# Performance work log

Measured on AMD Instinct MI355X. Metric: run time of the kernel, lower is better.

Reference implementation:

```python
import jax, jax.numpy as jnp
import numpy as np

B, L, D, H = 2, 2048, 1024, 16
HD = D // H
NEG = -1000000000.0


def setup_inputs() -> dict:
    key = jax.random.key(0)
    ks = jax.random.split(key, 11)
    s = 1.0 / np.sqrt(D)
    return {
        "q": jax.random.normal(ks[0], (B, L, D), jnp.float32),
        "k": jax.random.normal(ks[1], (B, L, D), jnp.float32),
        "v": jax.random.normal(ks[2], (B, L, D), jnp.float32),
        "mask": jnp.ones((B, L, L), jnp.int32),
        "Wq": jax.random.normal(ks[3], (D, D), jnp.float32) * s,
        "bq": jnp.zeros((D,), jnp.float32),
        "Wk": jax.random.normal(ks[4], (D, D), jnp.float32) * s,
        "bk": jnp.zeros((D,), jnp.float32),
        "Wv": jax.random.normal(ks[5], (D, D), jnp.float32) * s,
        "bv": jnp.zeros((D,), jnp.float32),
        "Wo": jax.random.normal(ks[6], (D, D), jnp.float32) * s,
        "bo": jnp.zeros((D,), jnp.float32),
    }


def _split(x):
    # [B,L,D] -> [B,H,L,HD]
    return x.reshape(B, L, H, HD).transpose(0, 2, 1, 3)


def reference(q, k, v, mask, Wq, bq, Wk, bk, Wv, bv, Wo, bo):
    Q = _split(q @ Wq.T + bq)
    K = _split(k @ Wk.T + bk)
    V = _split(v @ Wv.T + bv)
    scores = jnp.einsum("bhqd,bhkd->bhqk", Q, K) / jnp.sqrt(jnp.float32(HD))
    m = mask[:, None, :, :]  # [B,1,L,L]
    scores = jnp.where(m == 0, NEG, scores)
    attn = jax.nn.softmax(scores, axis=-1)
    out = jnp.einsum("bhqk,bhkd->bhqd", attn, V)
    out = out.transpose(0, 2, 1, 3).reshape(B, L, D)
    out = out @ Wo.T + bo
    return out, attn
```

## Files before the change

kernel.cpp:

```cpp
#include <hip/hip_runtime.h>
#include <stdint.h>

#define BSZ 2
#define LSEQ 2048
#define DMOD 1024
#define NH 16
#define HDSZ 64
#define NT (LSEQ / 128)

typedef __attribute__((ext_vector_type(8))) short short8;
typedef __attribute__((ext_vector_type(4))) float f32x4;
typedef __attribute__((ext_vector_type(4))) unsigned short u16x4;
typedef __attribute__((ext_vector_type(4))) int i32x4;

#define MFMA16(a, b, c) __builtin_amdgcn_mfma_f32_16x16x32_bf16((a), (b), (c), 0, 0, 0)
#define EXP2F(x) __builtin_amdgcn_exp2f(x)

__device__ __forceinline__ unsigned short f2bf(float f) {
  union { float f; unsigned u; } x; x.f = f;
  unsigned u = x.u + 0x7fffu + ((x.u >> 16) & 1u);
  return (unsigned short)(u >> 16);
}

__device__ __forceinline__ unsigned cvt_pk_bf16(float lo, float hi) {
  unsigned r;
  asm("v_cvt_pk_bf16_f32 %0, %1, %2" : "=v"(r) : "v"(lo), "v"(hi));
  return r;
}

__device__ __forceinline__ short8 pack8(f32x4 lo, f32x4 hi) {
  short8 o;
  o[0] = f2bf(lo[0]); o[1] = f2bf(lo[1]); o[2] = f2bf(lo[2]); o[3] = f2bf(lo[3]);
  o[4] = f2bf(hi[0]); o[5] = f2bf(hi[1]); o[6] = f2bf(hi[2]); o[7] = f2bf(hi[3]);
  return o;
}

template <int AF32, int OUTF32>
__global__ __launch_bounds__(256) void gemm_bt(
    const void* __restrict__ A0, const void* __restrict__ A1, const void* __restrict__ A2,
    const float* __restrict__ W0, const float* __restrict__ W1, const float* __restrict__ W2,
    const float* __restrict__ b0, const float* __restrict__ b1, const float* __restrict__ b2,
    void* __restrict__ C0, void* __restrict__ C1, void* __restrict__ C2,
    float s0, float s1, float s2, int vtz, int M, int N, int K,
    const int* __restrict__ mask, int* __restrict__ flags) {
  const int z = blockIdx.z;
  const int tid = threadIdx.x;
  __shared__ int red[4];

  if (z == 3) {
    const int t0 = (blockIdx.x + 32 * blockIdx.y) * 2;
#pragma unroll
    for (int t = t0; t < t0 + 2; ++t) {
      const int b_ = t >> 8, qt = (t >> 4) & 15, ktt = t & 15;
      const int r = tid >> 1, c = (tid & 1) * 64;
      const int* mr = mask + (size_t)b_ * LSEQ * LSEQ + (size_t)(qt * 128 + r) * LSEQ +
                      ktt * 128 + c;
      int ok = 1;
#pragma unroll
      for (int j = 0; j < 16; j++) {
        i32x4 v = __builtin_nontemporal_load((const i32x4*)(mr + j * 4));
        ok &= (v[0] != 0) & (v[1] != 0) & (v[2] != 0) & (v[3] != 0);
      }
      unsigned long long vote = __ballot(ok);
      if ((tid & 63) == 0) red[tid >> 6] = (vote == ~0ull) ? 1 : 0;
      __syncthreads();
      if (tid == 0) flags[(b_ * 16 + qt) * 16 + ktt] = red[0] & red[1] & red[2] & red[3];
      __syncthreads();
    }
    return;
  }

  const void* A = (z == 0) ? A0 : ((z == 1) ? A1 : A2);
  const float* W = (z == 0) ? W0 : ((z == 1) ? W1 : W2);
  const float* bias = (z == 0) ? b0 : ((z == 1) ? b1 : b2);
  void* Cout = (z == 0) ? C0 : ((z == 1) ? C1 : C2);
  const float scale = (z == 0) ? s0 : ((z == 1) ? s1 : s2);

  __shared__ unsigned short As[128 * 40];
  __shared__ unsigned short Bs[128 * 40];

  const int lane = tid & 63;
  const int wid = tid >> 6;
  const int bm = blockIdx.x, bn = blockIdx.y;
  const int wm = (wid >> 1) * 64, wn = (wid & 1) * 64;

  f32x4 acc[4][4];
#pragma unroll
  for (int i = 0; i < 4; i++)
#pragma unroll
    for (int j = 0; j < 4; j++) acc[i][j] = (f32x4){0.f, 0.f, 0.f, 0.f};

  const int r0 = tid >> 2;
  const int c0 = (tid & 3) * 8;
  const float* Wg = W + (size_t)(bn * 128 + r0) * K + c0;

  f32x4 vaf[2][2], vbf[2][2];
  short8 vah[2];
  if constexpr (AF32) {
    const float* Ag = (const float*)A + (size_t)(bm * 128 + r0) * K + c0;
#pragma unroll
    for (int j = 0; j < 2; j++) {
      vaf[j][0] = *(const f32x4*)(Ag + (size_t)(j * 64) * K);
      vaf[j][1] = *(const f32x4*)(Ag + (size_t)(j * 64) * K + 4);
    }
  } else {
    const unsigned short* Ag = (const unsigned short*)A + (size_t)(bm * 128 + r0) * K + c0;
#pragma unroll
    for (int j = 0; j < 2; j++) vah[j] = *(const short8*)(Ag + (size_t)(j * 64) * K);
  }
#pragma unroll
  for (int j = 0; j < 2; j++) {
    vbf[j][0] = *(const f32x4*)(Wg + (size_t)(j * 64) * K);
    vbf[j][1] = *(const f32x4*)(Wg + (size_t)(j * 64) * K + 4);
  }

  for (int k0 = 0; k0 < K; k0 += 32) {
#pragma unroll
    for (int j = 0; j < 2; j++) {
      if constexpr (AF32)
        *(short8*)&As[(j * 64 + r0) * 40 + c0] = pack8(vaf[j][0], vaf[j][1]);
      else
        *(short8*)&As[(j * 64 + r0) * 40 + c0] = vah[j];
      *(short8*)&Bs[(j * 64 + r0) * 40 + c0] = pack8(vbf[j][0], vbf[j][1]);
    }
    __syncthreads();
    if (k0 + 32 < K) {
      if constexpr (AF32) {
        const float* Ag = (const float*)A + (size_t)(bm * 128 + r0) * K + c0 + k0 + 32;
#pragma unroll
        for (int j = 0; j < 2; j++) {
          vaf[j][0] = *(const f32x4*)(Ag + (size_t)(j * 64) * K);
          vaf[j][1] = *(const f32x4*)(Ag + (size_t)(j * 64) * K + 4);
        }
      } else {
        const unsigned short* Ag =
            (const unsigned short*)A + (size_t)(bm * 128 + r0) * K + c0 + k0 + 32;
#pragma unroll
        for (int j = 0; j < 2; j++) vah[j] = *(const short8*)(Ag + (size_t)(j * 64) * K);
      }
#pragma unroll
      for (int j = 0; j < 2; j++) {
        vbf[j][0] = *(const f32x4*)(Wg + (size_t)(j * 64) * K + k0 + 32);
        vbf[j][1] = *(const f32x4*)(Wg + (size_t)(j * 64) * K + k0 + 36);
      }
    }
    short8 af[4], bf[4];
#pragma unroll
    for (int i = 0; i < 4; i++)
      af[i] = *(const short8*)&As[(wm + i * 16 + (lane & 15)) * 40 + (lane >> 4) * 8];
#pragma unroll
    for (int i = 0; i < 4; i++)
      bf[i] = *(const short8*)&Bs[(wn + i * 16 + (lane & 15)) * 40 + (lane >> 4) * 8];
#pragma unroll
    for (int i = 0; i < 4; i++)
#pragma unroll
      for (int j = 0; j < 4; j++) acc[i][j] = MFMA16(af[i], bf[j], acc[i][j]);
    __syncthreads();
  }

  const bool vtrans = (z == vtz);
  const int crow = bm * 128 + wm + ((lane >> 4) & 3) * 4;
#pragma unroll
  for (int j = 0; j < 4; j++) {
    const int col = bn * 128 + wn + j * 16 + (lane & 15);
    const float bv = bias[col];
#pragma unroll
    for (int i = 0; i < 4; i++) {
      if (OUTF32) {
#pragma unroll
        for (int r = 0; r < 4; r++) {
          float vvv = (acc[i][j][r] + bv) * scale;
          ((float*)Cout)[(size_t)(crow + i * 16 + r) * N + col] = vvv;
        }
      } else if (vtrans) {
        u16x4 pk;
#pragma unroll
        for (int r = 0; r < 4; r++) pk[r] = f2bf((acc[i][j][r] + bv) * scale);
        const int row = crow + i * 16;
        unsigned short* dst = (unsigned short*)Cout +
                              (size_t)(row >> 11) * DMOD * LSEQ + (size_t)col * LSEQ +
                              (row & (LSEQ - 1));
        *(u16x4*)dst = pk;
      } else {
#pragma unroll
        for (int r = 0; r < 4; r++) {
          float vvv = (acc[i][j][r] + bv) * scale;
          ((unsigned short*)Cout)[(size_t)(crow + i * 16 + r) * N + col] = f2bf(vvv);
        }
      }
    }
  }
}

__global__ __launch_bounds__(256) void attn_kernel(
    const unsigned short* __restrict__ Qp, const unsigned short* __restrict__ Kp,
    const unsigned short* __restrict__ Vt, const int* __restrict__ mask,
    const int* __restrict__ flags, float* __restrict__ attn_out,
    unsigned short* __restrict__ ctx) {
  __shared__ unsigned short Ks[4][64 * 64];
  __shared__ unsigned short Ps[4][64][68];
  __shared__ float denbuf[2][128];

  const int tid = threadIdx.x, lane = tid & 63, wid = tid >> 6;
  const int kw = wid & 1, qw = wid >> 1;
  const int l15 = lane & 15, lg = lane >> 4;

  const int wgid = blockIdx.x + gridDim.x * blockIdx.y;
  const int jj = wgid >> 3;
  const int bh = (wgid & 7) * 4 + (jj >> 4);
  const int qt = jj & 15;
  const int q0 = qt * 128;
  const int b = bh >> 4, h = bh & 15;

  const unsigned short* Qh = Qp + (size_t)b * LSEQ * DMOD + h * HDSZ;
  const unsigned short* Kh = Kp + (size_t)b * LSEQ * DMOD + h * HDSZ;
  const unsigned short* Vh = Vt + (size_t)b * DMOD * LSEQ + (size_t)h * HDSZ * LSEQ;
  const int* mb = mask + (size_t)b * LSEQ * LSEQ;
  const int* frow = flags + (b * 16 + qt) * 16;
  float* ah = attn_out + (size_t)bh * LSEQ * LSEQ;

  const int wq0 = q0 + qw * 64;
  const int wk0 = kw * 64;

  short8 qf[4][2];
#pragma unroll
  for (int fq = 0; fq < 4; fq++)
#pragma unroll
    for (int ks = 0; ks < 2; ks++)
      qf[fq][ks] = *(const short8*)(Qh + (size_t)(wq0 + fq * 16 + l15) * DMOD +
                                    ks * 32 + lg * 8);

  unsigned short* Ksw = &Ks[wid][0];
  const int rl8 = lane >> 3, jc = lane & 7;
  const unsigned short* Kwb = Kh + (size_t)(wk0 + rl8) * DMOD + jc * 8;

  float den[4] = {0.f, 0.f, 0.f, 0.f};
  short8 ka[8];
#pragma unroll
  for (int p = 0; p < 8; p++) ka[p] = *(const short8*)(Kwb + (size_t)(p * 8) * DMOD);

  for (int kt = 0; kt < NT; ++kt) {
#pragma unroll
    for (int p = 0; p < 8; p++) {
      const int r = p * 8 + rl8;
      *(short8*)&Ksw[r * 64 + ((jc ^ (r & 7)) << 3)] = ka[p];
    }
    if (kt + 1 < NT) {
#pragma unroll
      for (int p = 0; p < 8; p++)
        ka[p] = *(const short8*)(Kwb + (size_t)((kt + 1) * 128 + p * 8) * DMOD);
    }
    const bool fast = frow[kt] != 0;
    if (fast) {
#pragma unroll
      for (int fn = 0; fn < 4; fn++) {
        const int krow = fn * 16 + l15;
        const int rb = krow * 64, rx = (krow & 7) << 4;
        short8 kf0 = *(const short8*)&Ksw[rb + (((lg * 16) ^ rx) >> 1)];
        short8 kf1 = *(const short8*)&Ksw[rb + (((64 + lg * 16) ^ rx) >> 1)];
#pragma unroll
        for (int fq = 0; fq < 4; fq++) {
          f32x4 s = (f32x4){0.f, 0.f, 0.f, 0.f};
          s = MFMA16(kf0, qf[fq][0], s);
          s = MFMA16(kf1, qf[fq][1], s);
          den[fq] += EXP2F(s[0]) + EXP2F(s[1]) + EXP2F(s[2]) + EXP2F(s[3]);
        }
      }
    } else {
      const int k0 = kt * 128;
#pragma unroll
      for (int fn = 0; fn < 4; fn++) {
        const int krow = fn * 16 + l15;
        const int rb = krow * 64, rx = (krow & 7) << 4;
        short8 kf0 = *(const short8*)&Ksw[rb + (((lg * 16) ^ rx) >> 1)];
        short8 kf1 = *(const short8*)&Ksw[rb + (((64 + lg * 16) ^ rx) >> 1)];
#pragma unroll
        for (int fq = 0; fq < 4; fq++) {
          const int qrow = wq0 + fq * 16 + l15;
          f32x4 s = (f32x4){0.f, 0.f, 0.f, 0.f};
          s = MFMA16(kf0, qf[fq][0], s);
          s = MFMA16(kf1, qf[fq][1], s);
          i32x4 m4 = *(const i32x4*)(mb + (size_t)qrow * LSEQ + k0 + wk0 + fn * 16 + lg * 4);
          den[fq] += (m4[0] != 0) ? EXP2F(s[0]) : 0.f;
          den[fq] += (m4[1] != 0) ? EXP2F(s[1]) : 0.f;
          den[fq] += (m4[2] != 0) ? EXP2F(s[2]) : 0.f;
          den[fq] += (m4[3] != 0) ? EXP2F(s[3]) : 0.f;
        }
      }
    }
  }
#pragma unroll
  for (int fq = 0; fq < 4; fq++) {
    den[fq] += __shfl_xor(den[fq], 16);
    den[fq] += __shfl_xor(den[fq], 32);
  }
  if (lg == 0) {
#pragma unroll
    for (int fq = 0; fq < 4; fq++) denbuf[kw][qw * 64 + fq * 16 + l15] = den[fq];
  }
  __syncthreads();
  float inv[4];
#pragma unroll
  for (int fq = 0; fq < 4; fq++) {
    const int ql = qw * 64 + fq * 16 + l15;
    inv[fq] = 1.0f / (denbuf[0][ql] + denbuf[1][ql]);
  }

  f32x4 oacc[4][4];
#pragma unroll
  for (int fq = 0; fq < 4; fq++)
#pragma unroll
    for (int fd = 0; fd < 4; fd++) oacc[fq][fd] = (f32x4){0.f, 0.f, 0.f, 0.f};

#pragma unroll
  for (int p = 0; p < 8; p++) ka[p] = *(const short8*)(Kwb + (size_t)(p * 8) * DMOD);

  const unsigned short* Vbase = Vh + (size_t)l15 * LSEQ + wk0 + lg * 8;

  for (int kt = 0; kt < NT; ++kt) {
    const int k0 = kt * 128;
#pragma unroll
    for (int p = 0; p < 8; p++) {
      const int r = p * 8 + rl8;
      *(short8*)&Ksw[r * 64 + ((jc ^ (r & 7)) << 3)] = ka[p];
    }
    if (kt + 1 < NT) {
#pragma unroll
      for (int p = 0; p < 8; p++)
        ka[p] = *(const short8*)(Kwb + (size_t)((kt + 1) * 128 + p * 8) * DMOD);
    }
    short8 vf[4][2];
#pragma unroll
    for (int fd = 0; fd < 4; fd++)
#pragma unroll
      for (int ks = 0; ks < 2; ks++)
        vf[fd][ks] = *(const short8*)(Vbase + (size_t)(fd * 16) * LSEQ + k0 + ks * 32);

    const bool fast = frow[kt] != 0;
    if (fast) {
#pragma unroll
      for (int fn = 0; fn < 4; fn++) {
        const int krow = fn * 16 + l15;
        const int rb = krow * 64, rx = (krow & 7) << 4;
        short8 kf0 = *(const short8*)&Ksw[rb + (((lg * 16) ^ rx) >> 1)];
        short8 kf1 = *(const short8*)&Ksw[rb + (((64 + lg * 16) ^ rx) >> 1)];
#pragma unroll
        for (int fq = 0; fq < 4; fq++) {
          f32x4 s = (f32x4){0.f, 0.f, 0.f, 0.f};
          s = MFMA16(kf0, qf[fq][0], s);
          s = MFMA16(kf1, qf[fq][1], s);
          f32x4 a;
          a[0] = EXP2F(s[0]) * inv[fq];
          a[1] = EXP2F(s[1]) * inv[fq];
          a[2] = EXP2F(s[2]) * inv[fq];
          a[3] = EXP2F(s[3]) * inv[fq];
          union { u16x4 pk; unsigned u[2]; } P;
          P.u[0] = cvt_pk_bf16(a[0], a[1]);
          P.u[1] = cvt_pk_bf16(a[2], a[3]);
          *(u16x4*)&Ps[wid][fq * 16 + l15][fn * 16 + lg * 4] = P.pk;
        }
      }
    } else {
#pragma unroll
      for (int fn = 0; fn < 4; fn++) {
        const int krow = fn * 16 + l15;
        const int rb = krow * 64, rx = (krow & 7) << 4;
        short8 kf0 = *(const short8*)&Ksw[rb + (((lg * 16) ^ rx) >> 1)];
        short8 kf1 = *(const short8*)&Ksw[rb + (((64 + lg * 16) ^ rx) >> 1)];
#pragma unroll
        for (int fq = 0; fq < 4; fq++) {
          const int qrow = wq0 + fq * 16 + l15;
          f32x4 s = (f32x4){0.f, 0.f, 0.f, 0.f};
          s = MFMA16(kf0, qf[fq][0], s);
          s = MFMA16(kf1, qf[fq][1], s);
          i32x4 m4 = *(const i32x4*)(mb + (size_t)qrow * LSEQ + k0 + wk0 + fn * 16 + lg * 4);
          f32x4 a;
          a[0] = (m4[0] != 0) ? EXP2F(s[0]) * inv[fq] : 0.f;
          a[1] = (m4[1] != 0) ? EXP2F(s[1]) * inv[fq] : 0.f;
          a[2] = (m4[2] != 0) ? EXP2F(s[2]) * inv[fq] : 0.f;
          a[3] = (m4[3] != 0) ? EXP2F(s[3]) * inv[fq] : 0.f;
          union { u16x4 pk; unsigned u[2]; } P;
          P.u[0] = cvt_pk_bf16(a[0], a[1]);
          P.u[1] = cvt_pk_bf16(a[2], a[3]);
          *(u16x4*)&Ps[wid][fq * 16 + l15][fn * 16 + lg * 4] = P.pk;
        }
      }
    }
    short8 pa2[4][2];
#pragma unroll
    for (int fq = 0; fq < 4; fq++)
#pragma unroll
      for (int ks = 0; ks < 2; ks++)
        pa2[fq][ks] = *(const short8*)&Ps[wid][fq * 16 + l15][ks * 32 + lg * 8];
#pragma unroll
    for (int fd = 0; fd < 4; fd++) {
#pragma unroll
      for (int fq = 0; fq < 4; fq++) {
        oacc[fq][fd] = MFMA16(pa2[fq][0], vf[fd][0], oacc[fq][fd]);
        oacc[fq][fd] = MFMA16(pa2[fq][1], vf[fd][1], oacc[fq][fd]);
      }
    }
    {
      float* abase = ah + (size_t)wq0 * LSEQ + k0 + wk0;
#pragma unroll
      for (int i = 0; i < 16; i++) {
        const int qoff = i * 4 + lg;
        unsigned long long d = *(const unsigned long long*)&Ps[wid][qoff][l15 * 4];
        unsigned d0 = (unsigned)d, d1 = (unsigned)(d >> 32);
        union { unsigned u; float f; } t0, t1, t2, t3;
        t0.u = d0 << 16;
        t1.u = d0 & 0xffff0000u;
        t2.u = d1 << 16;
        t3.u = d1 & 0xffff0000u;
        f32x4 a = (f32x4){t0.f, t1.f, t2.f, t3.f};
        __builtin_nontemporal_store(a, (f32x4*)(abase + (size_t)qoff * LSEQ + l15 * 4));
      }
    }
  }

  __syncthreads();
  float* red = (float*)&Ps[qw * 2][0][0];
  if (kw == 1) {
#pragma unroll
    for (int fq = 0; fq < 4; fq++)
#pragma unroll
      for (int fd = 0; fd < 4; fd++)
#pragma unroll
        for (int r = 0; r < 4; r++)
          red[(fq * 16 + lg * 4 + r) * 65 + fd * 16 + l15] = oacc[fq][fd][r];
  }
  __syncthreads();
  if (kw == 0) {
    unsigned short* ch = ctx + (size_t)b * LSEQ * DMOD + h * HDSZ;
#pragma unroll
    for (int fq = 0; fq < 4; fq++)
#pragma unroll
      for (int fd = 0; fd < 4; fd++)
#pragma unroll
        for (int r = 0; r < 4; r++) {
          const int qr = wq0 + fq * 16 + lg * 4 + r;
          const float o = oacc[fq][fd][r] + red[(fq * 16 + lg * 4 + r) * 65 + fd * 16 + l15];
          ch[(size_t)qr * DMOD + fd * 16 + l15] = f2bf(o);
        }
  }
}

extern "C" void kernel_launch(void* const* d_in, const int* in_sizes, int n_in,
                              void* d_out, int out_size, void* d_ws, size_t ws_size,
                              hipStream_t stream) {
  const float* q = (const float*)d_in[0];
  const float* k = (const float*)d_in[1];
  const float* v = (const float*)d_in[2];
  const int* mask = (const int*)d_in[3];
  const float* Wq = (const float*)d_in[4];
  const float* bq = (const float*)d_in[5];
  const float* Wk = (const float*)d_in[6];
  const float* bk = (const float*)d_in[7];
  const float* Wv = (const float*)d_in[8];
  const float* bv = (const float*)d_in[9];
  const float* Wo = (const float*)d_in[10];
  const float* bo = (const float*)d_in[11];

  float* out = (float*)d_out;
  float* attn = out + (size_t)BSZ * LSEQ * DMOD;

  const size_t NQKV = (size_t)BSZ * LSEQ * DMOD;

  int* flags = (int*)out;

  unsigned short* Qp = (unsigned short*)d_ws;
  unsigned short* Kp = Qp + NQKV;
  unsigned short* Vt = Kp + NQKV;
  unsigned short* ctx = Vt + NQKV;

  gemm_bt<1, 0><<<dim3(32, 8, 4), 256, 0, stream>>>(
      q, k, v, Wq, Wk, Wv, bq, bk, bv, (void*)Qp, (void*)Kp, (void*)Vt,
      0.18033688011112042f, 1.0f, 1.0f, 2, BSZ * LSEQ, DMOD, DMOD, mask, flags);

  attn_kernel<<<dim3(LSEQ / 128, BSZ * NH), 256, 0, stream>>>(Qp, Kp, Vt, mask, flags,
                                                              attn, ctx);

  gemm_bt<0, 1><<<dim3(32, 8, 1), 256, 0, stream>>>(
      ctx, ctx, ctx, Wo, Wo, Wo, bo, bo, bo, (void*)out, (void*)out, (void*)out,
      1.0f, 1.0f, 1.0f, -1, BSZ * LSEQ, DMOD, DMOD, nullptr, nullptr);
}
```

Before: 238.2 us.

## Load GEMM tiles via direct global-to-LDS with XOR swizzle, convert at fragment read

```diff
diff --git a/kernel.cpp b/kernel.cpp
--- a/kernel.cpp
+++ b/kernel.cpp
@@ -28,11 +28,18 @@
   return r;
 }
 
-__device__ __forceinline__ short8 pack8(f32x4 lo, f32x4 hi) {
-  short8 o;
-  o[0] = f2bf(lo[0]); o[1] = f2bf(lo[1]); o[2] = f2bf(lo[2]); o[3] = f2bf(lo[3]);
-  o[4] = f2bf(hi[0]); o[5] = f2bf(hi[1]); o[6] = f2bf(hi[2]); o[7] = f2bf(hi[3]);
-  return o;
+__device__ __forceinline__ short8 pack8_pk(f32x4 lo, f32x4 hi) {
+  union { short8 s; unsigned u[4]; } r;
+  r.u[0] = cvt_pk_bf16(lo[0], lo[1]);
+  r.u[1] = cvt_pk_bf16(lo[2], lo[3]);
+  r.u[2] = cvt_pk_bf16(hi[0], hi[1]);
+  r.u[3] = cvt_pk_bf16(hi[2], hi[3]);
+  return r.s;
+}
+
+__device__ __forceinline__ void gll16(const void* src, void* lds) {
+  __builtin_amdgcn_global_load_lds((const __attribute__((address_space(1))) void*)src,
+                                   (__attribute__((address_space(3))) void*)lds, 16, 0, 0);
 }
 
 template <int AF32, int OUTF32>
@@ -76,13 +83,16 @@
   void* Cout = (z == 0) ? C0 : ((z == 1) ? C1 : C2);
   const float scale = (z == 0) ? s0 : ((z == 1) ? s1 : s2);
 
-  __shared__ unsigned short As[128 * 40];
-  __shared__ unsigned short Bs[128 * 40];
+  __shared__ __align__(16) float smem[AF32 ? 8192 : 6144];
+  float* Bs32 = smem;
+  float* As32 = smem + 4096;
+  unsigned short* As16 = (unsigned short*)(smem + 4096);
 
   const int lane = tid & 63;
   const int wid = tid >> 6;
   const int bm = blockIdx.x, bn = blockIdx.y;
   const int wm = (wid >> 1) * 64, wn = (wid & 1) * 64;
+  const int l15 = lane & 15, lg = lane >> 4;
 
   f32x4 acc[4][4];
 #pragma unroll
@@ -90,67 +100,59 @@
 #pragma unroll
     for (int j = 0; j < 4; j++) acc[i][j] = (f32x4){0.f, 0.f, 0.f, 0.f};
 
-  const int r0 = tid >> 2;
-  const int c0 = (tid & 3) * 8;
-  const float* Wg = W + (size_t)(bn * 128 + r0) * K + c0;
-
-  f32x4 vaf[2][2], vbf[2][2];
-  short8 vah[2];
-  if constexpr (AF32) {
-    const float* Ag = (const float*)A + (size_t)(bm * 128 + r0) * K + c0;
-#pragma unroll
-    for (int j = 0; j < 2; j++) {
-      vaf[j][0] = *(const f32x4*)(Ag + (size_t)(j * 64) * K);
-      vaf[j][1] = *(const f32x4*)(Ag + (size_t)(j * 64) * K + 4);
-    }
-  } else {
-    const unsigned short* Ag = (const unsigned short*)A + (size_t)(bm * 128 + r0) * K + c0;
-#pragma unroll
-    for (int j = 0; j < 2; j++) vah[j] = *(const short8*)(Ag + (size_t)(j * 64) * K);
-  }
-#pragma unroll
-  for (int j = 0; j < 2; j++) {
-    vbf[j][0] = *(const f32x4*)(Wg + (size_t)(j * 64) * K);
-    vbf[j][1] = *(const f32x4*)(Wg + (size_t)(j * 64) * K + 4);
-  }
+  const int r8 = lane >> 3, c8 = lane & 7;
+  const int r4 = lane >> 2, c4 = lane & 3;
+
+  const float* Wg = W + (size_t)(bn * 128) * K;
+  const float* Ag32 = (const float*)A + (size_t)(bm * 128) * K;
+  const unsigned short* Ag16 = (const unsigned short*)A + (size_t)(bm * 128) * K;
 
   for (int k0 = 0; k0 < K; k0 += 32) {
 #pragma unroll
-    for (int j = 0; j < 2; j++) {
-      if constexpr (AF32)
-        *(short8*)&As[(j * 64 + r0) * 40 + c0] = pack8(vaf[j][0], vaf[j][1]);
-      else
-        *(short8*)&As[(j * 64 + r0) * 40 + c0] = vah[j];
-      *(short8*)&Bs[(j * 64 + r0) * 40 + c0] = pack8(vbf[j][0], vbf[j][1]);
+    for (int gi = 0; gi < 4; gi++) {
+      const int g = wid * 4 + gi;
+      const int row = g * 8 + r8;
+      const int ch = c8 ^ (row & 7);
+      gll16(Wg + (size_t)row * K + k0 + ch * 4, Bs32 + g * 256);
+    }
+    if constexpr (AF32) {
+#pragma unroll
+      for (int gi = 0; gi < 4; gi++) {
+        const int g = wid * 4 + gi;
+        const int row = g * 8 + r8;
+        const int ch = c8 ^ (row & 7);
+        gll16(Ag32 + (size_t)row * K + k0 + ch * 4, As32 + g * 256);
+      }
+    } else {
+#pragma unroll
+      for (int gi = 0; gi < 2; gi++) {
+        const int g = wid * 2 + gi;
+        const int row = g * 16 + r4;
+        const int ch = c4 ^ (row & 3);
+        gll16(Ag16 + (size_t)row * K + k0 + ch * 8, As16 + g * 512);
+      }
     }
     __syncthreads();
-    if (k0 + 32 < K) {
+
+    short8 af[4], bf[4];
+#pragma unroll
+    for (int i = 0; i < 4; i++) {
+      const int row = wm + i * 16 + l15;
       if constexpr (AF32) {
-        const float* Ag = (const float*)A + (size_t)(bm * 128 + r0) * K + c0 + k0 + 32;
-#pragma unroll
-        for (int j = 0; j < 2; j++) {
-          vaf[j][0] = *(const f32x4*)(Ag + (size_t)(j * 64) * K);
-          vaf[j][1] = *(const f32x4*)(Ag + (size_t)(j * 64) * K + 4);
-        }
+        f32x4 lo = *(const f32x4*)&As32[row * 32 + (((2 * lg) ^ (row & 7)) << 2)];
+        f32x4 hi = *(const f32x4*)&As32[row * 32 + (((2 * lg + 1) ^ (row & 7)) << 2)];
+        af[i] = pack8_pk(lo, hi);
       } else {
-        const unsigned short* Ag =
-            (const unsigned short*)A + (size_t)(bm * 128 + r0) * K + c0 + k0 + 32;
-#pragma unroll
-        for (int j = 0; j < 2; j++) vah[j] = *(const short8*)(Ag + (size_t)(j * 64) * K);
-      }
-#pragma unroll
-      for (int j = 0; j < 2; j++) {
-        vbf[j][0] = *(const f32x4*)(Wg + (size_t)(j * 64) * K + k0 + 32);
-        vbf[j][1] = *(const f32x4*)(Wg + (size_t)(j * 64) * K + k0 + 36);
-      }
-    }
-    short8 af[4], bf[4];
-#pragma unroll
-    for (int i = 0; i < 4; i++)
-      af[i] = *(const short8*)&As[(wm + i * 16 + (lane & 15)) * 40 + (lane >> 4) * 8];
-#pragma unroll
-    for (int i = 0; i < 4; i++)
-      bf[i] = *(const short8*)&Bs[(wn + i * 16 + (lane & 15)) * 40 + (lane >> 4) * 8];
+        af[i] = *(const short8*)&As16[row * 32 + ((lg ^ (row & 3)) << 3)];
+      }
+    }
+#pragma unroll
+    for (int j = 0; j < 4; j++) {
+      const int row = wn + j * 16 + l15;
+      f32x4 lo = *(const f32x4*)&Bs32[row * 32 + (((2 * lg) ^ (row & 7)) << 2)];
+      f32x4 hi = *(const f32x4*)&Bs32[row * 32 + (((2 * lg + 1) ^ (row & 7)) << 2)];
+      bf[j] = pack8_pk(lo, hi);
+    }
 #pragma unroll
     for (int i = 0; i < 4; i++)
 #pragma unroll
```

Result: slower. 252.2 us (+5.9%).
